# Performance work log

Hardware: AMD Instinct MI355X
Metric: run time of the kernel (lower is better)

The kernel has to match this reference:

```python
import jax, jax.numpy as jnp
import numpy as np

N_NODES = 50000
N_EDGES = 1600000
IN_FEATS = 256
OUT_FEATS = 64


def setup_inputs() -> dict:
    key = jax.random.key(0)
    k_x, k_w, k_b, k_s, k_d = jax.random.split(key, 5)
    x = jax.random.normal(k_x, (N_NODES, IN_FEATS), dtype=jnp.float32)
    # nn.Linear(in_feats, out_feats): weight [out, in], bias [out]
    W = jax.random.normal(k_w, (OUT_FEATS, IN_FEATS), dtype=jnp.float32) / np.sqrt(IN_FEATS)
    b = jax.random.normal(k_b, (OUT_FEATS,), dtype=jnp.float32) * 0.01
    edge_src = jax.random.randint(k_s, (N_EDGES,), 0, N_NODES, dtype=jnp.int32)
    edge_dst = jax.random.randint(k_d, (N_EDGES,), 0, N_NODES, dtype=jnp.int32)
    return {"x": x, "W": W, "b": b, "edge_src": edge_src, "edge_dst": edge_dst}


def reference(x, W, b, edge_src, edge_dst):
    # h = dropout(relu(Linear(x)))  -- dropout p=0 (eval) => identity
    h = jax.nn.relu(x @ W.T + b)                     # [N, out_feats]
    # update_all: message = h[src], reduce = mean over incoming edges per dst
    msg = h[edge_src]                                # [E, out_feats] gather
    summed = jax.ops.segment_sum(msg, edge_dst, num_segments=N_NODES)  # [N, out]
    deg = jax.ops.segment_sum(jnp.ones((edge_src.shape[0],), dtype=h.dtype),
                              edge_dst, num_segments=N_NODES)          # [N]
    deg = jnp.maximum(deg, 1.0)
    return summed / deg[:, None]
```

## Files before the change

kernel.cpp:

```cpp
#include <hip/hip_runtime.h>
#include <hip/hip_bf16.h>

#define K_IN 256
#define O_OUT 64
#define NBINS 1024
#define NPB 49
#define CAP 1824
#define PART_CHUNK 4096

typedef __attribute__((ext_vector_type(8))) short short8;
typedef __attribute__((ext_vector_type(4))) float f32x4;

__device__ inline unsigned short bf16bits(float a) {
  __hip_bfloat16 t = __float2bfloat16(a);
  return *(unsigned short*)&t;
}

__device__ inline short8 cvt8(float4 f0, float4 f1) {
  short8 r;
  r[0] = (short)bf16bits(f0.x); r[1] = (short)bf16bits(f0.y);
  r[2] = (short)bf16bits(f0.z); r[3] = (short)bf16bits(f0.w);
  r[4] = (short)bf16bits(f1.x); r[5] = (short)bf16bits(f1.y);
  r[6] = (short)bf16bits(f1.z); r[7] = (short)bf16bits(f1.w);
  return r;
}

__global__ __launch_bounds__(256) void k_prep(const float* __restrict__ W,
                                              unsigned short* __restrict__ Wb,
                                              int* __restrict__ cursor) {
  int i = blockIdx.x * 256 + threadIdx.x;
  Wb[i] = bf16bits(W[i]);
  if (i < NBINS) cursor[i] = 0;
}

struct GemmSmem {
  unsigned short wsb[64 * 256];
};
struct PartSmem {
  int cnt[NBINS];
  int scanb[NBINS];
  int gbase[NBINS];
  int wsum[4];
  unsigned ord[PART_CHUNK];
};
union FusedSmem {
  GemmSmem g;
  PartSmem p;
};

__device__ void gemm_body(GemmSmem& sm, int gid, const float* __restrict__ x,
                          const unsigned short* __restrict__ Wb,
                          const float* __restrict__ bias,
                          __hip_bfloat16* __restrict__ h, int N) {
  const int tid = threadIdx.x;
  const int lane = tid & 63;
  const int wv = tid >> 6;
  const int n0 = gid * 64;

  {
    const uint4* wsrc = (const uint4*)Wb;
#pragma unroll
    for (int r = 0; r < 8; ++r) {
      int flat = r * 256 + tid;
      int row = flat >> 5;
      int c16 = flat & 31;
      unsigned byte = (unsigned)(row * 512 + c16 * 16);
      byte ^= (unsigned)((row & 7) << 4);
      *(uint4*)((char*)sm.wsb + byte) = wsrc[flat];
    }
  }

  f32x4 acc[4] = {{0.f, 0.f, 0.f, 0.f}, {0.f, 0.f, 0.f, 0.f},
                  {0.f, 0.f, 0.f, 0.f}, {0.f, 0.f, 0.f, 0.f}};

  int anode = n0 + wv * 16 + (lane & 15);
  if (anode > N - 1) anode = N - 1;
  const float* aptr = x + (size_t)anode * K_IN + (lane >> 4) * 8;
  const int brow0 = lane & 15;
  const unsigned kb = (unsigned)((lane >> 4) * 16);
  const unsigned bswz = (unsigned)((brow0 & 7) << 4);

  __syncthreads();

#pragma unroll
  for (int k = 0; k < K_IN; k += 32) {
    float4 f0 = *(const float4*)(aptr + k);
    float4 f1 = *(const float4*)(aptr + k + 4);
    short8 a = cvt8(f0, f1);
#pragma unroll
    for (int nt = 0; nt < 4; ++nt) {
      unsigned byte = (unsigned)((brow0 + nt * 16) * 512 + k * 2) + kb;
      byte ^= bswz;
      short8 bfr = *(const short8*)((const char*)sm.wsb + byte);
      acc[nt] = __builtin_amdgcn_mfma_f32_16x16x32_bf16(a, bfr, acc[nt], 0, 0, 0);
    }
  }

  const int col = lane & 15;
  const int rbase = (lane >> 4) * 4;
#pragma unroll
  for (int nt = 0; nt < 4; ++nt) {
    float bv = bias[nt * 16 + col];
#pragma unroll
    for (int j = 0; j < 4; ++j) {
      int node = n0 + wv * 16 + rbase + j;
      if (node < N) {
        float v = fmaxf(acc[nt][j] + bv, 0.f);
        h[(size_t)node * O_OUT + nt * 16 + col] = __float2bfloat16(v);
      }
    }
  }
}

__device__ void part_body(PartSmem& sm, int pid, const int* __restrict__ esrc,
                          const int* __restrict__ edst, int* __restrict__ cursor,
                          unsigned* __restrict__ bucket, int E) {
  const int tid = threadIdx.x;
  const int lane = tid & 63;
  const int wid = tid >> 6;
  const int base = pid * PART_CHUNK;

#pragma unroll
  for (int r = 0; r < 4; ++r) sm.cnt[r * 256 + tid] = 0;
  __syncthreads();

  unsigned pk[16];
  int bn[16];
  int rk[16];
#pragma unroll
  for (int r = 0; r < 4; ++r) {
    int e0 = base + r * 1024 + tid * 4;
    int4 s4, d4;
    if (e0 + 3 < E) {
      s4 = *(const int4*)(esrc + e0);
      d4 = *(const int4*)(edst + e0);
    } else {
      s4 = make_int4(0, 0, 0, 0);
      d4 = make_int4(0, 0, 0, 0);
      int* sp = (int*)&s4;
      int* dp = (int*)&d4;
      for (int j = 0; j < 4; ++j)
        if (e0 + j < E) { sp[j] = esrc[e0 + j]; dp[j] = edst[e0 + j]; }
    }
    const int* sp = (const int*)&s4;
    const int* dp = (const int*)&d4;
#pragma unroll
    for (int j = 0; j < 4; ++j) {
      int k = r * 4 + j;
      int e = e0 + j;
      if (e < E) {
        int s = sp[j];
        int d = dp[j];
        int bb = (int)__umulhi((unsigned)d, 87652394u);
        int dl = d - bb * NPB;
        pk[k] = (unsigned)s | ((unsigned)dl << 16) | ((unsigned)bb << 22);
        bn[k] = bb;
        rk[k] = atomicAdd(&sm.cnt[bb], 1);
      } else {
        bn[k] = -1;
      }
    }
  }
  __syncthreads();

  int c0 = sm.cnt[4 * tid];
  int c1 = sm.cnt[4 * tid + 1];
  int c2 = sm.cnt[4 * tid + 2];
  int c3 = sm.cnt[4 * tid + 3];
  int s = c0 + c1 + c2 + c3;
  int incl = s;
#pragma unroll
  for (int off = 1; off < 64; off <<= 1) {
    int t = __shfl_up(incl, off);
    if (lane >= off) incl += t;
  }
  if (lane == 63) sm.wsum[wid] = incl;
  __syncthreads();
  int wpre = 0;
  for (int w = 0; w < wid; ++w) wpre += sm.wsum[w];
  int excl = wpre + incl - s;
  sm.scanb[4 * tid] = excl;
  sm.scanb[4 * tid + 1] = excl + c0;
  sm.scanb[4 * tid + 2] = excl + c0 + c1;
  sm.scanb[4 * tid + 3] = excl + c0 + c1 + c2;
  sm.gbase[4 * tid] = (c0 > 0) ? atomicAdd(&cursor[4 * tid], c0) : 0;
  sm.gbase[4 * tid + 1] = (c1 > 0) ? atomicAdd(&cursor[4 * tid + 1], c1) : 0;
  sm.gbase[4 * tid + 2] = (c2 > 0) ? atomicAdd(&cursor[4 * tid + 2], c2) : 0;
  sm.gbase[4 * tid + 3] = (c3 > 0) ? atomicAdd(&cursor[4 * tid + 3], c3) : 0;
  __syncthreads();

#pragma unroll
  for (int k = 0; k < 16; ++k) {
    if (bn[k] >= 0) {
      int pos = sm.scanb[bn[k]] + rk[k];
      sm.ord[pos] = pk[k];
    }
  }
  __syncthreads();

  int nv = E - base;
  if (nv > PART_CHUNK) nv = PART_CHUNK;
  for (int p = tid; p < nv; p += 256) {
    unsigned v = sm.ord[p];
    int bb = v >> 22;
    int slot = sm.gbase[bb] + (p - sm.scanb[bb]);
    if (slot < CAP) bucket[(size_t)bb * CAP + slot] = v;
  }
}

__global__ __launch_bounds__(256, 5) void k_fused(const float* __restrict__ x,
                                                  const unsigned short* __restrict__ Wb,
                                                  const float* __restrict__ bias,
                                                  __hip_bfloat16* __restrict__ h,
                                                  const int* __restrict__ esrc,
                                                  const int* __restrict__ edst,
                                                  int* __restrict__ cursor,
                                                  unsigned* __restrict__ bucket,
                                                  int N, int E) {
  __shared__ FusedSmem sm;
  const int npart = (E + PART_CHUNK - 1) / PART_CHUNK;
  const int b = blockIdx.x;
  if (b % 3 == 1 && b / 3 < npart) {
    part_body(sm.p, b / 3, esrc, edst, cursor, bucket, E);
  } else {
    int skipped = (b + 2) / 3;
    if (skipped > npart) skipped = npart;
    gemm_body(sm.g, b - skipped, x, Wb, bias, h, N);
  }
}

__global__ __launch_bounds__(512) void k_sortagg(const unsigned* __restrict__ bucket,
                                                 const int* __restrict__ cursor,
                                                 const unsigned* __restrict__ h32,
                                                 float* __restrict__ out, int N) {
  __shared__ int hist[NPB];
  __shared__ int offs[NPB];
  __shared__ unsigned short sbuf[CAP + 64];

  const int tid = threadIdx.x;
  const int lane = tid & 63;
  const int wid = tid >> 6;
  const int bin = blockIdx.x;

  if (tid < NPB) hist[tid] = 0;
  __syncthreads();

  int cnt = cursor[bin];
  if (cnt > CAP) cnt = CAP;
  const unsigned* bb = bucket + (size_t)bin * CAP;

  unsigned pk[4];
  int rk[4];
  {
    int i0 = tid * 4;
    uint4 v;
    if (i0 + 3 < cnt) {
      v = *(const uint4*)(bb + i0);
    } else {
      v = make_uint4(0, 0, 0, 0);
      unsigned* vp = (unsigned*)&v;
      for (int j = 0; j < 4; ++j)
        if (i0 + j < cnt) vp[j] = bb[i0 + j];
    }
    const unsigned* vp = (const unsigned*)&v;
#pragma unroll
    for (int j = 0; j < 4; ++j) {
      if (i0 + j < cnt) {
        pk[j] = vp[j];
        rk[j] = atomicAdd(&hist[(vp[j] >> 16) & 63], 1);
      } else {
        rk[j] = -1;
      }
    }
  }
  __syncthreads();

  if (tid < 64) {
    int hval = (tid < NPB) ? hist[tid] : 0;
    int incl = hval;
#pragma unroll
    for (int off = 1; off < 64; off <<= 1) {
      int t = __shfl_up(incl, off);
      if (lane >= off) incl += t;
    }
    if (tid < NPB) offs[tid] = incl - hval;
  }
  __syncthreads();

#pragma unroll
  for (int j = 0; j < 4; ++j) {
    if (rk[j] >= 0)
      sbuf[offs[(pk[j] >> 16) & 63] + rk[j]] = (unsigned short)(pk[j] & 0xFFFFu);
  }
  __syncthreads();

  const int q = lane >> 4;
  const int hl = lane & 15;
  const uint2* __restrict__ h2 = (const uint2*)h32;

  for (int nl = wid; nl < NPB; nl += 8) {
    int n = bin * NPB + nl;
    if (n >= N) break;
    int c = hist[nl];
    const unsigned short* bs = sbuf + offs[nl];

    float a0 = 0.f, a1 = 0.f, a2 = 0.f, a3 = 0.f;
    const int nqc = (c + 3) >> 2;
    for (int i0 = 0; i0 < nqc; i0 += 8) {
      int p[8];
#pragma unroll
      for (int k = 0; k < 8; ++k) {
        int e = (i0 + k) * 4 + q;
        p[k] = (e < c) ? (int)bs[e] : 0;
      }
#pragma unroll
      for (int k = 0; k < 8; ++k) {
        float wk = ((i0 + k) * 4 + q < c) ? 1.f : 0.f;
        uint2 u = h2[p[k] * 16 + hl];
        a0 = fmaf(wk, __uint_as_float(u.x << 16), a0);
        a1 = fmaf(wk, __uint_as_float(u.x & 0xFFFF0000u), a1);
        a2 = fmaf(wk, __uint_as_float(u.y << 16), a2);
        a3 = fmaf(wk, __uint_as_float(u.y & 0xFFFF0000u), a3);
      }
    }

    a0 += __shfl_xor(a0, 16); a1 += __shfl_xor(a1, 16);
    a2 += __shfl_xor(a2, 16); a3 += __shfl_xor(a3, 16);
    a0 += __shfl_xor(a0, 32); a1 += __shfl_xor(a1, 32);
    a2 += __shfl_xor(a2, 32); a3 += __shfl_xor(a3, 32);

    if (lane < 16) {
      float inv = 1.f / fmaxf((float)c, 1.f);
      float4 r;
      r.x = a0 * inv; r.y = a1 * inv; r.z = a2 * inv; r.w = a3 * inv;
      *(float4*)(out + (size_t)n * O_OUT + hl * 4) = r;
    }
  }
}

extern "C" void kernel_launch(void* const* d_in, const int* in_sizes, int n_in,
                              void* d_out, int out_size, void* d_ws, size_t ws_size,
                              hipStream_t stream) {
  const float* x = (const float*)d_in[0];
  const float* W = (const float*)d_in[1];
  const float* b = (const float*)d_in[2];
  const int* esrc = (const int*)d_in[3];
  const int* edst = (const int*)d_in[4];
  float* out = (float*)d_out;

  const int N = in_sizes[0] / K_IN;
  const int E = in_sizes[3];

  char* ws = (char*)d_ws;
  unsigned short* Wb = (unsigned short*)ws;
  __hip_bfloat16* h = (__hip_bfloat16*)(ws + 32768);
  size_t off = 32768 + (size_t)N * O_OUT * sizeof(__hip_bfloat16);
  int* cursor = (int*)(ws + off);
  off += NBINS * sizeof(int);
  unsigned* bucket = (unsigned*)(ws + off);

  const int ngemm = (N + 63) / 64;
  const int npart = (E + PART_CHUNK - 1) / PART_CHUNK;

  k_prep<<<(K_IN * O_OUT) / 256, 256, 0, stream>>>(W, Wb, cursor);
  k_fused<<<ngemm + npart, 256, 0, stream>>>(x, Wb, b, h, esrc, edst, cursor,
                                             bucket, N, E);
  k_sortagg<<<NBINS, 512, 0, stream>>>(bucket, cursor, (const unsigned*)h, out, N);
}
```

Measured before the change: 160.8 us.

## Batch loads in gemm, partition and aggregation; halve sortagg block size

The GEMM body now handles 128 nodes per block, loading the whole A row strip into registers before the MFMA loop, and staging the W copy through registers. The partition body issues all edge loads before the shared-memory barrier. Block interleaving changes to alternate gemm and partition blocks. The aggregation kernel drops to 256 threads: each warp processes two nodes at once and issues 12 gathers per node before accumulating, with a tail loop for high-degree nodes. The aim is more memory-level parallelism and less latency stall, at the cost of more registers and lower occupancy.

Measured after the change: 160.8 us. About the same (+0.0%).

```diff
diff --git a/kernel.cpp b/kernel.cpp
--- a/kernel.cpp
+++ b/kernel.cpp
@@ -55,10 +55,12 @@
   const int tid = threadIdx.x;
   const int lane = tid & 63;
   const int wv = tid >> 6;
-  const int n0 = gid * 64;
 
   {
     const uint4* wsrc = (const uint4*)Wb;
+    uint4 wtmp[8];
+#pragma unroll
+    for (int r = 0; r < 8; ++r) wtmp[r] = wsrc[r * 256 + tid];
 #pragma unroll
     for (int r = 0; r < 8; ++r) {
       int flat = r * 256 + tid;
@@ -66,47 +68,55 @@
       int c16 = flat & 31;
       unsigned byte = (unsigned)(row * 512 + c16 * 16);
       byte ^= (unsigned)((row & 7) << 4);
-      *(uint4*)((char*)sm.wsb + byte) = wsrc[flat];
-    }
-  }
-
-  f32x4 acc[4] = {{0.f, 0.f, 0.f, 0.f}, {0.f, 0.f, 0.f, 0.f},
-                  {0.f, 0.f, 0.f, 0.f}, {0.f, 0.f, 0.f, 0.f}};
-
-  int anode = n0 + wv * 16 + (lane & 15);
-  if (anode > N - 1) anode = N - 1;
-  const float* aptr = x + (size_t)anode * K_IN + (lane >> 4) * 8;
+      *(uint4*)((char*)sm.wsb + byte) = wtmp[r];
+    }
+  }
+  __syncthreads();
+
   const int brow0 = lane & 15;
   const unsigned kb = (unsigned)((lane >> 4) * 16);
   const unsigned bswz = (unsigned)((brow0 & 7) << 4);
 
-  __syncthreads();
-
-#pragma unroll
-  for (int k = 0; k < K_IN; k += 32) {
-    float4 f0 = *(const float4*)(aptr + k);
-    float4 f1 = *(const float4*)(aptr + k + 4);
-    short8 a = cvt8(f0, f1);
+#pragma unroll
+  for (int t = 0; t < 2; ++t) {
+    const int n0 = gid * 128 + t * 64;
+    int anode = n0 + wv * 16 + (lane & 15);
+    if (anode > N - 1) anode = N - 1;
+    const float* aptr = x + (size_t)anode * K_IN + (lane >> 4) * 8;
+
+    float4 f[16];
+#pragma unroll
+    for (int k8 = 0; k8 < 8; ++k8) {
+      f[2 * k8] = *(const float4*)(aptr + k8 * 32);
+      f[2 * k8 + 1] = *(const float4*)(aptr + k8 * 32 + 4);
+    }
+
+    f32x4 acc[4] = {{0.f, 0.f, 0.f, 0.f}, {0.f, 0.f, 0.f, 0.f},
+                    {0.f, 0.f, 0.f, 0.f}, {0.f, 0.f, 0.f, 0.f}};
+#pragma unroll
+    for (int k8 = 0; k8 < 8; ++k8) {
+      short8 a = cvt8(f[2 * k8], f[2 * k8 + 1]);
+#pragma unroll
+      for (int nt = 0; nt < 4; ++nt) {
+        unsigned byte = (unsigned)((brow0 + nt * 16) * 512 + k8 * 64) + kb;
+        byte ^= bswz;
+        short8 bfr = *(const short8*)((const char*)sm.wsb + byte);
+        acc[nt] = __builtin_amdgcn_mfma_f32_16x16x32_bf16(a, bfr, acc[nt], 0, 0, 0);
+      }
+    }
+
+    const int col = lane & 15;
+    const int rbase = (lane >> 4) * 4;
 #pragma unroll
     for (int nt = 0; nt < 4; ++nt) {
-      unsigned byte = (unsigned)((brow0 + nt * 16) * 512 + k * 2) + kb;
-      byte ^= bswz;
-      short8 bfr = *(const short8*)((const char*)sm.wsb + byte);
-      acc[nt] = __builtin_amdgcn_mfma_f32_16x16x32_bf16(a, bfr, acc[nt], 0, 0, 0);
-    }
-  }
-
-  const int col = lane & 15;
-  const int rbase = (lane >> 4) * 4;
-#pragma unroll
-  for (int nt = 0; nt < 4; ++nt) {
-    float bv = bias[nt * 16 + col];
-#pragma unroll
-    for (int j = 0; j < 4; ++j) {
-      int node = n0 + wv * 16 + rbase + j;
-      if (node < N) {
-        float v = fmaxf(acc[nt][j] + bv, 0.f);
-        h[(size_t)node * O_OUT + nt * 16 + col] = __float2bfloat16(v);
+      float bv = bias[nt * 16 + col];
+#pragma unroll
+      for (int j = 0; j < 4; ++j) {
+        int node = n0 + wv * 16 + rbase + j;
+        if (node < N) {
+          float v = fmaxf(acc[nt][j] + bv, 0.f);
+          h[(size_t)node * O_OUT + nt * 16 + col] = __float2bfloat16(v);
+        }
       }
     }
   }
@@ -122,42 +132,43 @@
 
 #pragma unroll
   for (int r = 0; r < 4; ++r) sm.cnt[r * 256 + tid] = 0;
-  __syncthreads();
-
-  unsigned pk[16];
-  int bn[16];
-  int rk[16];
+
+  int4 s4[4], d4[4];
 #pragma unroll
   for (int r = 0; r < 4; ++r) {
     int e0 = base + r * 1024 + tid * 4;
-    int4 s4, d4;
     if (e0 + 3 < E) {
-      s4 = *(const int4*)(esrc + e0);
-      d4 = *(const int4*)(edst + e0);
+      s4[r] = *(const int4*)(esrc + e0);
+      d4[r] = *(const int4*)(edst + e0);
     } else {
-      s4 = make_int4(0, 0, 0, 0);
-      d4 = make_int4(0, 0, 0, 0);
-      int* sp = (int*)&s4;
-      int* dp = (int*)&d4;
+      s4[r] = make_int4(0, 0, 0, 0);
+      d4[r] = make_int4(0, 0, 0, 0);
+      int* sp = (int*)&s4[r];
+      int* dp = (int*)&d4[r];
       for (int j = 0; j < 4; ++j)
         if (e0 + j < E) { sp[j] = esrc[e0 + j]; dp[j] = edst[e0 + j]; }
     }
-    const int* sp = (const int*)&s4;
-    const int* dp = (const int*)&d4;
+  }
+  __syncthreads();
+
+  unsigned pk[16];
+  int rk[16];
+#pragma unroll
+  for (int r = 0; r < 4; ++r) {
+    const int* sp = (const int*)&s4[r];
+    const int* dp = (const int*)&d4[r];
 #pragma unroll
     for (int j = 0; j < 4; ++j) {
       int k = r * 4 + j;
-      int e = e0 + j;
+      int e = base + r * 1024 + tid * 4 + j;
       if (e < E) {
-        int s = sp[j];
         int d = dp[j];
         int bb = (int)__umulhi((unsigned)d, 87652394u);
         int dl = d - bb * NPB;
-        pk[k] = (unsigned)s | ((unsigned)dl << 16) | ((unsigned)bb << 22);
-        bn[k] = bb;
+        pk[k] = (unsigned)sp[j] | ((unsigned)dl << 16) | ((unsigned)bb << 22);
         rk[k] = atomicAdd(&sm.cnt[bb], 1);
       } else {
-        bn[k] = -1;
+        rk[k] = -1;
       }
     }
   }
@@ -191,8 +202,9 @@
 
 #pragma unroll
   for (int k = 0; k < 16; ++k) {
-    if (bn[k] >= 0) {
-      int pos = sm.scanb[bn[k]] + rk[k];
+    if (rk[k] >= 0) {
+      int bb = (int)(pk[k] >> 22);
+      int pos = sm.scanb[bb] + rk[k];
       sm.ord[pos] = pk[k];
     }
   }
@@ -208,7 +220,7 @@
   }
 }
 
-__global__ __launch_bounds__(256, 5) void k_fused(const float* __restrict__ x,
+__global__ __launch_bounds__(256, 4) void k_fused(const float* __restrict__ x,
                                                   const unsigned short* __restrict__ Wb,
                                                   const float* __restrict__ bias,
                                                   __hip_bfloat16* __restrict__ h,
@@ -218,21 +230,24 @@
                                                   unsigned* __restrict__ bucket,
                                                   int N, int E) {
   __shared__ FusedSmem sm;
+  const int ngemm2 = (N + 127) / 128;
   const int npart = (E + PART_CHUNK - 1) / PART_CHUNK;
+  const int m2 = ngemm2 < npart ? ngemm2 : npart;
   const int b = blockIdx.x;
-  if (b % 3 == 1 && b / 3 < npart) {
-    part_body(sm.p, b / 3, esrc, edst, cursor, bucket, E);
+  if (b < 2 * m2) {
+    if (b & 1) part_body(sm.p, b >> 1, esrc, edst, cursor, bucket, E);
+    else gemm_body(sm.g, b >> 1, x, Wb, bias, h, N);
   } else {
-    int skipped = (b + 2) / 3;
-    if (skipped > npart) skipped = npart;
-    gemm_body(sm.g, b - skipped, x, Wb, bias, h, N);
-  }
-}
-
-__global__ __launch_bounds__(512) void k_sortagg(const unsigned* __restrict__ bucket,
-                                                 const int* __restrict__ cursor,
-                                                 const unsigned* __restrict__ h32,
-                                                 float* __restrict__ out, int N) {
+    int idx = b - m2;
+    if (ngemm2 > npart) gemm_body(sm.g, idx, x, Wb, bias, h, N);
+    else part_body(sm.p, idx, esrc, edst, cursor, bucket, E);
+  }
+}
+
+__global__ __launch_bounds__(256, 4) void k_sortagg(const unsigned* __restrict__ bucket,
+                                                    const int* __restrict__ cursor,
+                                                    const unsigned* __restrict__ h32,
+                                                    float* __restrict__ out, int N) {
   __shared__ int hist[NPB];
   __shared__ int offs[NPB];
   __shared__ unsigned short sbuf[CAP + 64];
@@ -249,10 +264,11 @@
   if (cnt > CAP) cnt = CAP;
   const unsigned* bb = bucket + (size_t)bin * CAP;
 
-  unsigned pk[4];
-  int rk[4];
-  {
-    int i0 = tid * 4;
+  unsigned pk2[2][4];
+  int rk2[2][4];
+#pragma unroll
+  for (int g = 0; g < 2; ++g) {
+    int i0 = (g * 256 + tid) * 4;
     uint4 v;
     if (i0 + 3 < cnt) {
       v = *(const uint4*)(bb + i0);
@@ -266,10 +282,10 @@
 #pragma unroll
     for (int j = 0; j < 4; ++j) {
       if (i0 + j < cnt) {
-        pk[j] = vp[j];
-        rk[j] = atomicAdd(&hist[(vp[j] >> 16) & 63], 1);
+        pk2[g][j] = vp[j];
+        rk2[g][j] = atomicAdd(&hist[(vp[j] >> 16) & 63], 1);
       } else {
-        rk[j] = -1;
+        rk2[g][j] = -1;
       }
     }
   }
@@ -288,10 +304,12 @@
   __syncthreads();
 
 #pragma unroll
-  for (int j = 0; j < 4; ++j) {
-    if (rk[j] >= 0)
-      sbuf[offs[(pk[j] >> 16) & 63] + rk[j]] = (unsigned short)(pk[j] & 0xFFFFu);
-  }
+  for (int g = 0; g < 2; ++g)
+#pragma unroll
+    for (int j = 0; j < 4; ++j)
+      if (rk2[g][j] >= 0)
+        sbuf[offs[(pk2[g][j] >> 16) & 63] + rk2[g][j]] =
+            (unsigned short)(pk2[g][j] & 0xFFFFu);
   __syncthreads();
 
   const int q = lane >> 4;
@@ -299,41 +317,90 @@
   const uint2* __restrict__ h2 = (const uint2*)h32;
 
   for (int nl = wid; nl < NPB; nl += 8) {
-    int n = bin * NPB + nl;
-    if (n >= N) break;
-    int c = hist[nl];
-    const unsigned short* bs = sbuf + offs[nl];
+    const int nlb = nl + 4;
+    const bool hasb = (nlb < NPB);
+    const int ca = hist[nl];
+    const int cb = hasb ? hist[nlb] : 0;
+    const unsigned short* bsa = sbuf + offs[nl];
+    const unsigned short* bsb = sbuf + (hasb ? offs[nlb] : 0);
+
+    int pa[12], pb[12];
+#pragma unroll
+    for (int k = 0; k < 12; ++k) {
+      int e = k * 4 + q;
+      pa[k] = (e < ca) ? (int)bsa[e] : 0;
+      pb[k] = (e < cb) ? (int)bsb[e] : 0;
+    }
+    uint2 ua[12], ub[12];
+#pragma unroll
+    for (int k = 0; k < 12; ++k) ua[k] = h2[(size_t)pa[k] * 16 + hl];
+#pragma unroll
+    for (int k = 0; k < 12; ++k) ub[k] = h2[(size_t)pb[k] * 16 + hl];
 
     float a0 = 0.f, a1 = 0.f, a2 = 0.f, a3 = 0.f;
-    const int nqc = (c + 3) >> 2;
-    for (int i0 = 0; i0 < nqc; i0 += 8) {
-      int p[8];
-#pragma unroll
-      for (int k = 0; k < 8; ++k) {
-        int e = (i0 + k) * 4 + q;
-        p[k] = (e < c) ? (int)bs[e] : 0;
-      }
-#pragma unroll
-      for (int k = 0; k < 8; ++k) {
-        float wk = ((i0 + k) * 4 + q < c) ? 1.f : 0.f;
-        uint2 u = h2[p[k] * 16 + hl];
-        a0 = fmaf(wk, __uint_as_float(u.x << 16), a0);
-        a1 = fmaf(wk, __uint_as_float(u.x & 0xFFFF0000u), a1);
-        a2 = fmaf(wk, __uint_as_float(u.y << 16), a2);
-        a3 = fmaf(wk, __uint_as_float(u.y & 0xFFFF0000u), a3);
-      }
+    float b0 = 0.f, b1 = 0.f, b2 = 0.f, b3 = 0.f;
+#pragma unroll
+    for (int k = 0; k < 12; ++k) {
+      float wk = (k * 4 + q < ca) ? 1.f : 0.f;
+      a0 = fmaf(wk, __uint_as_float(ua[k].x << 16), a0);
+      a1 = fmaf(wk, __uint_as_float(ua[k].x & 0xFFFF0000u), a1);
+      a2 = fmaf(wk, __uint_as_float(ua[k].y << 16), a2);
+      a3 = fmaf(wk, __uint_as_float(ua[k].y & 0xFFFF0000u), a3);
+    }
+#pragma unroll
+    for (int k = 0; k < 12; ++k) {
+      float wk = (k * 4 + q < cb) ? 1.f : 0.f;
+      b0 = fmaf(wk, __uint_as_float(ub[k].x << 16), b0);
+      b1 = fmaf(wk, __uint_as_float(ub[k].x & 0xFFFF0000u), b1);
+      b2 = fmaf(wk, __uint_as_float(ub[k].y << 16), b2);
+      b3 = fmaf(wk, __uint_as_float(ub[k].y & 0xFFFF0000u), b3);
+    }
+
+    for (int e0 = 48; e0 < ca; e0 += 4) {
+      int e = e0 + q;
+      float wk = (e < ca) ? 1.f : 0.f;
+      int p = (e < ca) ? (int)bsa[e] : 0;
+      uint2 u = h2[(size_t)p * 16 + hl];
+      a0 = fmaf(wk, __uint_as_float(u.x << 16), a0);
+      a1 = fmaf(wk, __uint_as_float(u.x & 0xFFFF0000u), a1);
+      a2 = fmaf(wk, __uint_as_float(u.y << 16), a2);
+      a3 = fmaf(wk, __uint_as_float(u.y & 0xFFFF0000u), a3);
+    }
+    for (int e0 = 48; e0 < cb; e0 += 4) {
+      int e = e0 + q;
+      float wk = (e < cb) ? 1.f : 0.f;
+      int p = (e < cb) ? (int)bsb[e] : 0;
+      uint2 u = h2[(size_t)p * 16 + hl];
+      b0 = fmaf(wk, __uint_as_float(u.x << 16), b0);
+      b1 = fmaf(wk, __uint_as_float(u.x & 0xFFFF0000u), b1);
+      b2 = fmaf(wk, __uint_as_float(u.y << 16), b2);
+      b3 = fmaf(wk, __uint_as_float(u.y & 0xFFFF0000u), b3);
     }
 
     a0 += __shfl_xor(a0, 16); a1 += __shfl_xor(a1, 16);
     a2 += __shfl_xor(a2, 16); a3 += __shfl_xor(a3, 16);
+    b0 += __shfl_xor(b0, 16); b1 += __shfl_xor(b1, 16);
+    b2 += __shfl_xor(b2, 16); b3 += __shfl_xor(b3, 16);
     a0 += __shfl_xor(a0, 32); a1 += __shfl_xor(a1, 32);
     a2 += __shfl_xor(a2, 32); a3 += __shfl_xor(a3, 32);
+    b0 += __shfl_xor(b0, 32); b1 += __shfl_xor(b1, 32);
+    b2 += __shfl_xor(b2, 32); b3 += __shfl_xor(b3, 32);
 
     if (lane < 16) {
-      float inv = 1.f / fmaxf((float)c, 1.f);
-      float4 r;
-      r.x = a0 * inv; r.y = a1 * inv; r.z = a2 * inv; r.w = a3 * inv;
-      *(float4*)(out + (size_t)n * O_OUT + hl * 4) = r;
+      int na = bin * NPB + nl;
+      if (na < N) {
+        float inv = 1.f / fmaxf((float)ca, 1.f);
+        float4 r;
+        r.x = a0 * inv; r.y = a1 * inv; r.z = a2 * inv; r.w = a3 * inv;
+        *(float4*)(out + (size_t)na * O_OUT + hl * 4) = r;
+      }
+      int nb = bin * NPB + nlb;
+      if (hasb && nb < N) {
+        float inv = 1.f / fmaxf((float)cb, 1.f);
+        float4 r;
+        r.x = b0 * inv; r.y = b1 * inv; r.z = b2 * inv; r.w = b3 * inv;
+        *(float4*)(out + (size_t)nb * O_OUT + hl * 4) = r;
+      }
     }
   }
 }
@@ -359,11 +426,11 @@
   off += NBINS * sizeof(int);
   unsigned* bucket = (unsigned*)(ws + off);
 
-  const int ngemm = (N + 63) / 64;
+  const int ngemm2 = (N + 127) / 128;
   const int npart = (E + PART_CHUNK - 1) / PART_CHUNK;
 
   k_prep<<<(K_IN * O_OUT) / 256, 256, 0, stream>>>(W, Wb, cursor);
-  k_fused<<<ngemm + npart, 256, 0, stream>>>(x, Wb, b, h, esrc, edst, cursor,
-                                             bucket, N, E);
-  k_sortagg<<<NBINS, 512, 0, stream>>>(bucket, cursor, (const unsigned*)h, out, N);
-}
+  k_fused<<<ngemm2 + npart, 256, 0, stream>>>(x, Wb, b, h, esrc, edst, cursor,
+                                              bucket, N, E);
+  k_sortagg<<<NBINS, 256, 0, stream>>>(bucket, cursor, (const unsigned*)h, out, N);
+}
```
